# Performance work log

Hardware: AMD Instinct MI355X
Metric: run time of the kernel (lower is better)

Reference implementation:

```python
import jax, jax.numpy as jnp
import numpy as np

B, T = 16, 8192
L, RC, DC, SC, EC, E, NC = 16, 32, 32, 256, 256, 100, 256


def conv1d(x, w, b, dilation=1):
    # x: [B, Cin, T], w: [Cout, Cin, K], b: [Cout]
    y = jax.lax.conv_general_dilated(
        x, w, window_strides=(1,), padding='VALID',
        rhs_dilation=(dilation,), dimension_numbers=('NCH', 'OIH', 'NCH'))
    return y + b[None, :, None]


def setup_inputs() -> dict:
    key = jax.random.key(0)
    ks = jax.random.split(key, 32)
    n = lambda k, shp: (jax.random.normal(k, shp) * 0.1).astype(jnp.float32)
    return dict(
        tokens=jax.random.randint(ks[0], (B, T), 0, NC),
        emb=n(ks[1], (NC, E)),
        init_w=n(ks[2], (RC, E, 1)), init_b=n(ks[3], (RC,)),
        dil_w=n(ks[4], (L, DC, RC, 2)), dil_b=n(ks[5], (L, DC)),
        filt_w=n(ks[6], (L, DC, DC, 2)), filt_b=n(ks[7], (L, DC)),
        gate_w=n(ks[8], (L, DC, DC, 2)), gate_b=n(ks[9], (L, DC)),
        res_w=n(ks[10], (L, RC, DC, 1)), res_b=n(ks[11], (L, RC)),
        skip_w=n(ks[12], (L, SC, DC, 1)), skip_b=n(ks[13], (L, SC)),
        end1_w=n(ks[14], (EC, SC, 1)), end1_b=n(ks[15], (EC,)),
        end2_w=n(ks[16], (EC, EC, 1)), end2_b=n(ks[17], (EC,)),
        fc1_w=n(ks[18], (128, 256)), fc1_b=n(ks[19], (128,)),
        fc2_w=n(ks[20], (128, 128)), fc2_b=n(ks[21], (128,)),
        fc3_w=n(ks[22], (64, 128)), fc3_b=n(ks[23], (64,)),
        fc4_w=n(ks[24], (NC, 64)), fc4_b=n(ks[25], (NC,)),
    )


def reference(tokens, emb, init_w, init_b, dil_w, dil_b, filt_w, filt_b,
              gate_w, gate_b, res_w, res_b, skip_w, skip_b,
              end1_w, end1_b, end2_w, end2_b,
              fc1_w, fc1_b, fc2_w, fc2_b, fc3_w, fc3_b, fc4_w, fc4_b):
    x = emb[tokens]                     # [B, T, E]
    x = jnp.transpose(x, (0, 2, 1))     # [B, E, T]
    x = conv1d(x, init_w, init_b)       # [B, RC, T]
    skip = None
    for i in range(L):
        d = 2 ** (i % 4)                # dilation resets each block of 4 layers
        xp = jnp.pad(x, ((0, 0), (0, 0), (d + 1, 0)))        # left pad d+1
        residual = conv1d(xp, dil_w[i], dil_b[i], dilation=d)  # [B, DC, T+1]
        f = jnp.tanh(conv1d(residual, filt_w[i], filt_b[i]))   # [B, DC, T]
        g = jax.nn.sigmoid(conv1d(residual, gate_w[i], gate_b[i]))
        x = f * g
        skip = conv1d(x, skip_w[i], skip_b[i])   # overwritten each layer (source bug, kept faithful)
        x = conv1d(x, res_w[i], res_b[i]) + residual[:, :, :-1]
    h = jax.nn.relu(conv1d(jax.nn.relu(skip), end1_w, end1_b))
    h = conv1d(h, end2_w, end2_b)       # [B, EC, T]
    h = h[:, :, -1]                     # [B, 256] last timestep only
    h = jax.nn.relu(h @ fc1_w.T + fc1_b)
    h = jax.nn.relu(h @ fc2_w.T + fc2_b)
    h = jax.nn.relu(h @ fc3_w.T + fc3_b)
    out = h @ fc4_w.T + fc4_b           # [B, NC]
    return out
```

## Files before the change

### kernel.cpp

```cpp
#include <hip/hip_runtime.h>


#define BB 16
#define TT 8192
#define LL 16
#define W0 77
#define NT 256

typedef __attribute__((ext_vector_type(8)))  short short8;
typedef __attribute__((ext_vector_type(16))) float float16;

#define MFMA_B16(a, b, c) __builtin_amdgcn_mfma_f32_32x32x16_bf16(a, b, c, 0, 0, 0)

__device__ __forceinline__ short f2bs(float f) {
  union { float ff; unsigned u; } v; v.ff = f;
  unsigned u = v.u;
  return (short)((u + 0x7FFFu + ((u >> 16) & 1u)) >> 16);
}
__device__ __forceinline__ float b2f(short h) {
  union { unsigned u; float f; } v;
  v.u = ((unsigned)(unsigned short)h) << 16; return v.f;
}
__device__ __forceinline__ float fast_sigmoid(float x) {
  return 1.f / (1.f + __expf(-x));
}
__device__ __forceinline__ float fast_tanh(float x) {
  return 2.f / (1.f + __expf(-2.f * x)) - 1.f;
}

__device__ __forceinline__ void afrag2(const short* src, int row, int kh, short8* out) {
  #pragma unroll
  for (int h = 0; h < 2; h++)
    out[h] = *(const short8*)&src[row * 32 + 16 * h + 8 * kh];
}
__device__ __forceinline__ void bfragL(const short* bw, int mat, int n, int kh, short8* out) {
  #pragma unroll
  for (int h = 0; h < 2; h++)
    out[h] = *(const short8*)&bw[((mat * 2 + h) * 64 + n * 2 + kh) * 8];
}

__global__ __launch_bounds__(NT) void wavenet_kernel(
    const int* __restrict__ tokens,
    const float* __restrict__ emb,
    const float* __restrict__ init_w, const float* __restrict__ init_b,
    const float* __restrict__ dil_w,  const float* __restrict__ dil_b,
    const float* __restrict__ filt_w, const float* __restrict__ filt_b,
    const float* __restrict__ gate_w, const float* __restrict__ gate_b,
    const float* __restrict__ res_w,  const float* __restrict__ res_b,
    const float* __restrict__ skip_w, const float* __restrict__ skip_b,
    const float* __restrict__ end1_w, const float* __restrict__ end1_b,
    const float* __restrict__ end2_w, const float* __restrict__ end2_b,
    const float* __restrict__ fc1_w,  const float* __restrict__ fc1_b,
    const float* __restrict__ fc2_w,  const float* __restrict__ fc2_b,
    const float* __restrict__ fc3_w,  const float* __restrict__ fc3_b,
    const float* __restrict__ fc4_w,  const float* __restrict__ fc4_b,
    float* __restrict__ out)
{
  __shared__ __align__(16) short bfw[2][7168];
  __shared__ float bias2[2][128];
  __shared__ float resbuf[76 * 32];
  __shared__ __align__(16) short xbuf_bf[W0 * 32];
  __shared__ __align__(16) short resbuf_bf[76 * 32];
  __shared__ __align__(16) short xmid_bf[76 * 32];
  __shared__ int   tok[W0];
  __shared__ float vecA[256], vecB[256];

  const int b    = blockIdx.x;
  const int tid  = threadIdx.x;
  const int lane = tid & 63;
  const int wv   = tid >> 6;
  const int m    = lane & 31;
  const int kh   = lane >> 5;
  const int g    = tid >> 5;
  const int cc   = tid & 31;

  float pw[7][4];
  float pb[4];

  float* iwT = (float*)&bfw[1][0];

  if (tid < W0) tok[tid] = tokens[b * TT + (TT - 1 - tid)];
  for (int idx = tid; idx < 100 * 32; idx += NT) {
    int e = idx >> 5, c2 = idx & 31;
    iwT[idx] = init_w[c2 * 100 + e];
  }
  if (tid < 32) vecA[tid] = init_b[tid];

  #pragma unroll
  for (int q = 0; q < 4; q++) {
    int rc = g + 8 * q;
    int base = cc * 32 + rc;
    pw[0][q] = dil_w[base * 2 + 0];
    pw[1][q] = dil_w[base * 2 + 1];
    pw[2][q] = filt_w[base * 2 + 0];
    pw[3][q] = filt_w[base * 2 + 1];
    pw[4][q] = gate_w[base * 2 + 0];
    pw[5][q] = gate_w[base * 2 + 1];
    pw[6][q] = res_w[base];
  }
  if (tid < 32) {
    pb[0] = dil_b[tid]; pb[1] = filt_b[tid];
    pb[2] = gate_b[tid]; pb[3] = res_b[tid];
  }
  __syncthreads();

  {
    const float bc = vecA[cc];
    for (int base0 = 0; base0 < W0; base0 += 32) {
      float acc[4] = {bc, bc, bc, bc};
      const float* er[4];
      #pragma unroll
      for (int j = 0; j < 4; j++) {
        int u = base0 + g + 8 * j; if (u > W0 - 1) u = W0 - 1;
        er[j] = emb + tok[u] * 100;
      }
      #pragma unroll 5
      for (int eq = 0; eq < 100; eq += 4) {
        float w0 = iwT[(eq+0)*32+cc], w1 = iwT[(eq+1)*32+cc];
        float w2 = iwT[(eq+2)*32+cc], w3 = iwT[(eq+3)*32+cc];
        #pragma unroll
        for (int j = 0; j < 4; j++) {
          float4 e4 = *(const float4*)(er[j] + eq);
          acc[j] += (w0 * e4.x + w1 * e4.y) + (w2 * e4.z + w3 * e4.w);
        }
      }
      #pragma unroll
      for (int j = 0; j < 4; j++) {
        int u = base0 + g + 8 * j;
        if (u < W0) xbuf_bf[u * 32 + cc] = f2bs(acc[j]);
      }
    }
  }
  #pragma unroll
  for (int mat = 0; mat < 7; mat++)
    #pragma unroll
    for (int q = 0; q < 4; q++)
      bfw[0][((mat * 2 + (q >> 1)) * 64 + cc * 2 + (q & 1)) * 8 + g] = f2bs(pw[mat][q]);
  if (tid < 32) {
    bias2[0][tid] = pb[0]; bias2[0][32+tid] = pb[1];
    bias2[0][64+tid] = pb[2]; bias2[0][96+tid] = pb[3];
  }
  __syncthreads();

  int Win = W0;
  for (int i = 0; i < LL; i++) {
    const int d = 1 << (i & 3);
    const int Wout = Win - d - 1;
    const int T1 = (Wout + 32) >> 5;
    const int T2 = (Wout + 31) >> 5;
    const short* bw = bfw[i & 1];
    const float* bs = bias2[i & 1];

    if (i + 1 < LL) {
      const int ii = i + 1;
      #pragma unroll
      for (int q = 0; q < 4; q++) {
        int rc = g + 8 * q;
        int base = (ii * 32 + cc) * 32 + rc;
        pw[0][q] = dil_w[base * 2 + 0];
        pw[1][q] = dil_w[base * 2 + 1];
        pw[2][q] = filt_w[base * 2 + 0];
        pw[3][q] = filt_w[base * 2 + 1];
        pw[4][q] = gate_w[base * 2 + 0];
        pw[5][q] = gate_w[base * 2 + 1];
        pw[6][q] = res_w[base];
      }
      if (tid < 32) {
        pb[0] = dil_b[ii * 32 + tid]; pb[1] = filt_b[ii * 32 + tid];
        pb[2] = gate_b[ii * 32 + tid]; pb[3] = res_b[ii * 32 + tid];
      }
    }

    if (wv < T1) {
      const int R = wv * 32;
      short8 bD0[2], bD1[2];
      bfragL(bw, 0, m, kh, bD0);
      bfragL(bw, 1, m, kh, bD1);
      int vra = R + m + d; if (vra > Win - 1) vra = Win - 1;
      int vrz = R + m;     if (vrz > Win - 1) vrz = Win - 1;
      short8 aA[2], aZ[2];
      afrag2(xbuf_bf, vra, kh, aA);
      afrag2(xbuf_bf, vrz, kh, aZ);
      float16 acc;
      const float bc = bs[m];
      #pragma unroll
      for (int r = 0; r < 16; r++) acc[r] = bc;
      acc = MFMA_B16(aA[0], bD0[0], acc);
      acc = MFMA_B16(aA[1], bD0[1], acc);
      acc = MFMA_B16(aZ[0], bD1[0], acc);
      acc = MFMA_B16(aZ[1], bD1[1], acc);
      #pragma unroll
      for (int r = 0; r < 16; r++) {
        int row = (r & 3) + 8 * (r >> 2) + 4 * kh;
        int vr = R + row;
        if (vr <= Wout) {
          resbuf[vr * 32 + m]    = acc[r];
          resbuf_bf[vr * 32 + m] = f2bs(acc[r]);
        }
      }
    }
    __syncthreads();

    if (wv < T2) {
      const int R = wv * 32;
      short8 bF0[2], bF1[2], bG0[2], bG1[2];
      bfragL(bw, 2, m, kh, bF0);
      bfragL(bw, 3, m, kh, bF1);
      bfragL(bw, 4, m, kh, bG0);
      bfragL(bw, 5, m, kh, bG1);
      int r1 = R + m + 1; if (r1 > Wout) r1 = Wout;
      int r0 = R + m;     if (r0 > Wout) r0 = Wout;
      short8 a1[2], a0[2];
      afrag2(resbuf_bf, r1, kh, a1);
      afrag2(resbuf_bf, r0, kh, a0);
      float16 accF, accG;
      const float bf = bs[32 + m], bg = bs[64 + m];
      #pragma unroll
      for (int r = 0; r < 16; r++) { accF[r] = bf; accG[r] = bg; }
      accF = MFMA_B16(a1[0], bF0[0], accF);
      accF = MFMA_B16(a1[1], bF0[1], accF);
      accF = MFMA_B16(a0[0], bF1[0], accF);
      accF = MFMA_B16(a0[1], bF1[1], accF);
      accG = MFMA_B16(a1[0], bG0[0], accG);
      accG = MFMA_B16(a1[1], bG0[1], accG);
      accG = MFMA_B16(a0[0], bG1[0], accG);
      accG = MFMA_B16(a0[1], bG1[1], accG);
      #pragma unroll
      for (int r = 0; r < 16; r++) {
        int row = (r & 3) + 8 * (r >> 2) + 4 * kh;
        int uf = R + row;
        if (uf < Wout)
          xmid_bf[uf * 32 + m] = f2bs(fast_tanh(accF[r]) * fast_sigmoid(accG[r]));
      }
      asm volatile("s_waitcnt lgkmcnt(0)" ::: "memory");

      short8 bR[2];
      bfragL(bw, 6, m, kh, bR);
      int rx = R + m; if (rx > Wout - 1) rx = Wout - 1;
      short8 aX[2];
      afrag2(xmid_bf, rx, kh, aX);
      float16 accX;
      const float br = bs[96 + m];
      #pragma unroll
      for (int r = 0; r < 16; r++) {
        int row = (r & 3) + 8 * (r >> 2) + 4 * kh;
        int rr = R + row + 1; if (rr > Wout) rr = Wout;
        accX[r] = br + resbuf[rr * 32 + m];
      }
      accX = MFMA_B16(aX[0], bR[0], accX);
      accX = MFMA_B16(aX[1], bR[1], accX);
      #pragma unroll
      for (int r = 0; r < 16; r++) {
        int row = (r & 3) + 8 * (r >> 2) + 4 * kh;
        int uf = R + row;
        if (uf < Wout) xbuf_bf[uf * 32 + m] = f2bs(accX[r]);
      }
    }

    if (i + 1 < LL) {
      short* bwN = bfw[(i + 1) & 1];
      #pragma unroll
      for (int mat = 0; mat < 7; mat++)
        #pragma unroll
        for (int q = 0; q < 4; q++)
          bwN[((mat * 2 + (q >> 1)) * 64 + cc * 2 + (q & 1)) * 8 + g] = f2bs(pw[mat][q]);
      if (tid < 32) {
        float* bN = bias2[(i + 1) & 1];
        bN[tid] = pb[0]; bN[32+tid] = pb[1]; bN[64+tid] = pb[2]; bN[96+tid] = pb[3];
      }
    }
    __syncthreads();
    Win = Wout;
  }

  {
    float acc = skip_b[15 * 256 + tid];
    const float* wr = skip_w + (15 * 256 + tid) * 32;
    #pragma unroll
    for (int k = 0; k < 32; k += 4) {
      float4 w = *(const float4*)&wr[k];
      acc += (w.x * b2f(xmid_bf[k])   + w.y * b2f(xmid_bf[k+1]))
           + (w.z * b2f(xmid_bf[k+2]) + w.w * b2f(xmid_bf[k+3]));
    }
    vecA[tid] = fmaxf(acc, 0.f);
  }
  __syncthreads();
  {
    const float* wr = end1_w + tid * 256;
    float a4[4] = {0.f, 0.f, 0.f, 0.f};
    #pragma unroll 4
    for (int k = 0; k < 256; k += 16) {
      #pragma unroll
      for (int q = 0; q < 4; q++) {
        float4 w = *(const float4*)&wr[k + 4 * q];
        a4[q] += (w.x * vecA[k+4*q] + w.y * vecA[k+4*q+1]) + (w.z * vecA[k+4*q+2] + w.w * vecA[k+4*q+3]);
      }
    }
    vecB[tid] = fmaxf(end1_b[tid] + (a4[0] + a4[1]) + (a4[2] + a4[3]), 0.f);
  }
  __syncthreads();
  {
    const float* wr = end2_w + tid * 256;
    float a4[4] = {0.f, 0.f, 0.f, 0.f};
    #pragma unroll 4
    for (int k = 0; k < 256; k += 16) {
      #pragma unroll
      for (int q = 0; q < 4; q++) {
        float4 w = *(const float4*)&wr[k + 4 * q];
        a4[q] += (w.x * vecB[k+4*q] + w.y * vecB[k+4*q+1]) + (w.z * vecB[k+4*q+2] + w.w * vecB[k+4*q+3]);
      }
    }
    vecA[tid] = end2_b[tid] + (a4[0] + a4[1]) + (a4[2] + a4[3]);
  }
  __syncthreads();
  if (tid < 128) {
    const float* wr = fc1_w + tid * 256;
    float a4[4] = {0.f, 0.f, 0.f, 0.f};
    #pragma unroll 4
    for (int k = 0; k < 256; k += 16) {
      #pragma unroll
      for (int q = 0; q < 4; q++) {
        float4 w = *(const float4*)&wr[k + 4 * q];
        a4[q] += (w.x * vecA[k+4*q] + w.y * vecA[k+4*q+1]) + (w.z * vecA[k+4*q+2] + w.w * vecA[k+4*q+3]);
      }
    }
    vecB[tid] = fmaxf(fc1_b[tid] + (a4[0] + a4[1]) + (a4[2] + a4[3]), 0.f);
  }
  __syncthreads();
  if (tid < 128) {
    const float* wr = fc2_w + tid * 128;
    float a4[4] = {0.f, 0.f, 0.f, 0.f};
    #pragma unroll 2
    for (int k = 0; k < 128; k += 16) {
      #pragma unroll
      for (int q = 0; q < 4; q++) {
        float4 w = *(const float4*)&wr[k + 4 * q];
        a4[q] += (w.x * vecB[k+4*q] + w.y * vecB[k+4*q+1]) + (w.z * vecB[k+4*q+2] + w.w * vecB[k+4*q+3]);
      }
    }
    vecA[tid] = fmaxf(fc2_b[tid] + (a4[0] + a4[1]) + (a4[2] + a4[3]), 0.f);
  }
  __syncthreads();
  if (tid < 64) {
    const float* wr = fc3_w + tid * 128;
    float a4[4] = {0.f, 0.f, 0.f, 0.f};
    #pragma unroll 2
    for (int k = 0; k < 128; k += 16) {
      #pragma unroll
      for (int q = 0; q < 4; q++) {
        float4 w = *(const float4*)&wr[k + 4 * q];
        a4[q] += (w.x * vecA[k+4*q] + w.y * vecA[k+4*q+1]) + (w.z * vecA[k+4*q+2] + w.w * vecA[k+4*q+3]);
      }
    }
    vecB[tid] = fmaxf(fc3_b[tid] + (a4[0] + a4[1]) + (a4[2] + a4[3]), 0.f);
  }
  __syncthreads();
  {
    const float* wr = fc4_w + tid * 64;
    float a4[4] = {0.f, 0.f, 0.f, 0.f};
    #pragma unroll
    for (int k = 0; k < 64; k += 16) {
      #pragma unroll
      for (int q = 0; q < 4; q++) {
        float4 w = *(const float4*)&wr[k + 4 * q];
        a4[q] += (w.x * vecB[k+4*q] + w.y * vecB[k+4*q+1]) + (w.z * vecB[k+4*q+2] + w.w * vecB[k+4*q+3]);
      }
    }
    out[b * 256 + tid] = fc4_b[tid] + (a4[0] + a4[1]) + (a4[2] + a4[3]);
  }
}

extern "C" void kernel_launch(void* const* d_in, const int* in_sizes, int n_in,
                              void* d_out, int out_size, void* d_ws, size_t ws_size,
                              hipStream_t stream) {
  wavenet_kernel<<<BB, NT, 0, stream>>>(
      (const int*)d_in[0],    (const float*)d_in[1],  (const float*)d_in[2],  (const float*)d_in[3],
      (const float*)d_in[4],  (const float*)d_in[5],  (const float*)d_in[6],  (const float*)d_in[7],
      (const float*)d_in[8],  (const float*)d_in[9],  (const float*)d_in[10], (const float*)d_in[11],
      (const float*)d_in[12], (const float*)d_in[13], (const float*)d_in[14], (const float*)d_in[15],
      (const float*)d_in[16], (const float*)d_in[17], (const float*)d_in[18], (const float*)d_in[19],
      (const float*)d_in[20], (const float*)d_in[21], (const float*)d_in[22], (const float*)d_in[23],
      (const float*)d_in[24], (const float*)d_in[25], (float*)d_out);
}
```

Baseline: 216.7 us.

## Process two batch rows per block, sharing the layer-weight staging

Each 512-thread block now handles two batch elements, one per 256-thread half, with per-batch shared buffers. The per-layer weight prefetch and bf16 staging are split across both halves, so each thread loads half as many weights. The fp32 residual buffer is dropped and the residual is read back from bf16, and the tail vectors reuse the x buffer. The cost is a grid of only 8 blocks instead of 16, which roughly halves parallelism on a latency-bound kernel, plus a small precision loss in the residual path.

```diff
diff --git a/kernel.cpp b/kernel.cpp
--- a/kernel.cpp
+++ b/kernel.cpp
@@ -5,7 +5,7 @@
 #define TT 8192
 #define LL 16
 #define W0 77
-#define NT 256
+#define NT 512
 
 typedef __attribute__((ext_vector_type(8)))  short short8;
 typedef __attribute__((ext_vector_type(16))) float float16;
@@ -33,13 +33,13 @@
   for (int h = 0; h < 2; h++)
     out[h] = *(const short8*)&src[row * 32 + 16 * h + 8 * kh];
 }
-__device__ __forceinline__ void bfragL(const short* bw, int mat, int n, int kh, short8* out) {
+__device__ __forceinline__ void bfragL(const short* bw, int mat, int lane, short8* out) {
   #pragma unroll
   for (int h = 0; h < 2; h++)
-    out[h] = *(const short8*)&bw[((mat * 2 + h) * 64 + n * 2 + kh) * 8];
-}
-
-__global__ __launch_bounds__(NT) void wavenet_kernel(
+    out[h] = *(const short8*)&bw[((mat * 2 + h) * 64 + lane) * 8];
+}
+
+__global__ __launch_bounds__(NT, 2) void wavenet_kernel(
     const int* __restrict__ tokens,
     const float* __restrict__ emb,
     const float* __restrict__ init_w, const float* __restrict__ init_b,
@@ -58,45 +58,46 @@
 {
   __shared__ __align__(16) short bfw[2][7168];
   __shared__ float bias2[2][128];
-  __shared__ float resbuf[76 * 32];
-  __shared__ __align__(16) short xbuf_bf[W0 * 32];
-  __shared__ __align__(16) short resbuf_bf[76 * 32];
-  __shared__ __align__(16) short xmid_bf[76 * 32];
-  __shared__ int   tok[W0];
-  __shared__ float vecA[256], vecB[256];
-
-  const int b    = blockIdx.x;
+  __shared__ __align__(16) short xbuf_bf[2][W0 * 32];
+  __shared__ __align__(16) short resbuf_bf[2][76 * 32];
+  __shared__ __align__(16) short xmid_bf[2][76 * 32];
+  __shared__ int tok[2][W0];
+
   const int tid  = threadIdx.x;
   const int lane = tid & 63;
-  const int wv   = tid >> 6;
+  const int bat  = tid >> 8;
+  const int twv  = (tid >> 6) & 3;
   const int m    = lane & 31;
   const int kh   = lane >> 5;
-  const int g    = tid >> 5;
-  const int cc   = tid & 31;
-
-  float pw[7][4];
+  const int tid2 = tid & 255;
+  const int cc   = tid2 & 31;
+  const int g2   = tid2 >> 5;
+  const int bglob = blockIdx.x * 2 + bat;
+
+  const int qh = bat;
+  float pw[7][2];
   float pb[4];
 
   float* iwT = (float*)&bfw[1][0];
 
-  if (tid < W0) tok[tid] = tokens[b * TT + (TT - 1 - tid)];
+  if (tid2 < W0) tok[bat][tid2] = tokens[bglob * TT + (TT - 1 - tid2)];
   for (int idx = tid; idx < 100 * 32; idx += NT) {
     int e = idx >> 5, c2 = idx & 31;
     iwT[idx] = init_w[c2 * 100 + e];
   }
-  if (tid < 32) vecA[tid] = init_b[tid];
+  if (tid < 32) bias2[0][96 + tid] = init_b[tid];
 
   #pragma unroll
-  for (int q = 0; q < 4; q++) {
-    int rc = g + 8 * q;
+  for (int qi = 0; qi < 2; qi++) {
+    int rc = g2 + 8 * (2 * qh + qi);
     int base = cc * 32 + rc;
-    pw[0][q] = dil_w[base * 2 + 0];
-    pw[1][q] = dil_w[base * 2 + 1];
-    pw[2][q] = filt_w[base * 2 + 0];
-    pw[3][q] = filt_w[base * 2 + 1];
-    pw[4][q] = gate_w[base * 2 + 0];
-    pw[5][q] = gate_w[base * 2 + 1];
-    pw[6][q] = res_w[base];
+    pw[0][qi] = dil_w[base * 2 + 0];
+    pw[1][qi] = dil_w[base * 2 + 1];
+    pw[2][qi] = filt_w[base * 2 + 0];
+    pw[3][qi] = filt_w[base * 2 + 1];
+    pw[4][qi] = gate_w[base * 2 + 0];
+    pw[5][qi] = gate_w[base * 2 + 1];
+    pw[6][qi] = res_w[base];
   }
   if (tid < 32) {
     pb[0] = dil_b[tid]; pb[1] = filt_b[tid];
@@ -105,14 +106,15 @@
   __syncthreads();
 
   {
-    const float bc = vecA[cc];
+    const float bc = bias2[0][96 + cc];
+    short* xb = xbuf_bf[bat];
     for (int base0 = 0; base0 < W0; base0 += 32) {
       float acc[4] = {bc, bc, bc, bc};
       const float* er[4];
       #pragma unroll
       for (int j = 0; j < 4; j++) {
-        int u = base0 + g + 8 * j; if (u > W0 - 1) u = W0 - 1;
-        er[j] = emb + tok[u] * 100;
+        int u = base0 + g2 + 8 * j; if (u > W0 - 1) u = W0 - 1;
+        er[j] = emb + tok[bat][u] * 100;
       }
       #pragma unroll 5
       for (int eq = 0; eq < 100; eq += 4) {
@@ -126,16 +128,16 @@
       }
       #pragma unroll
       for (int j = 0; j < 4; j++) {
-        int u = base0 + g + 8 * j;
-        if (u < W0) xbuf_bf[u * 32 + cc] = f2bs(acc[j]);
+        int u = base0 + g2 + 8 * j;
+        if (u < W0) xb[u * 32 + cc] = f2bs(acc[j]);
       }
     }
   }
   #pragma unroll
   for (int mat = 0; mat < 7; mat++)
     #pragma unroll
-    for (int q = 0; q < 4; q++)
-      bfw[0][((mat * 2 + (q >> 1)) * 64 + cc * 2 + (q & 1)) * 8 + g] = f2bs(pw[mat][q]);
+    for (int qi = 0; qi < 2; qi++)
+      bfw[0][((mat * 2 + qh) * 64 + qi * 32 + cc) * 8 + g2] = f2bs(pw[mat][qi]);
   if (tid < 32) {
     bias2[0][tid] = pb[0]; bias2[0][32+tid] = pb[1];
     bias2[0][64+tid] = pb[2]; bias2[0][96+tid] = pb[3];
@@ -143,6 +145,9 @@
   __syncthreads();
 
   int Win = W0;
+  short* xb = xbuf_bf[bat];
+  short* rb = resbuf_bf[bat];
+  short* xm = xmid_bf[bat];
   for (int i = 0; i < LL; i++) {
     const int d = 1 << (i & 3);
     const int Wout = Win - d - 1;
@@ -154,16 +159,16 @@
     if (i + 1 < LL) {
       const int ii = i + 1;
       #pragma unroll
-      for (int q = 0; q < 4; q++) {
-        int rc = g + 8 * q;
+      for (int qi = 0; qi < 2; qi++) {
+        int rc = g2 + 8 * (2 * qh + qi);
         int base = (ii * 32 + cc) * 32 + rc;
-        pw[0][q] = dil_w[base * 2 + 0];
-        pw[1][q] = dil_w[base * 2 + 1];
-        pw[2][q] = filt_w[base * 2 + 0];
-        pw[3][q] = filt_w[base * 2 + 1];
-        pw[4][q] = gate_w[base * 2 + 0];
-        pw[5][q] = gate_w[base * 2 + 1];
-        pw[6][q] = res_w[base];
+        pw[0][qi] = dil_w[base * 2 + 0];
+        pw[1][qi] = dil_w[base * 2 + 1];
+        pw[2][qi] = filt_w[base * 2 + 0];
+        pw[3][qi] = filt_w[base * 2 + 1];
+        pw[4][qi] = gate_w[base * 2 + 0];
+        pw[5][qi] = gate_w[base * 2 + 1];
+        pw[6][qi] = res_w[base];
       }
       if (tid < 32) {
         pb[0] = dil_b[ii * 32 + tid]; pb[1] = filt_b[ii * 32 + tid];
@@ -171,16 +176,16 @@
       }
     }
 
-    if (wv < T1) {
-      const int R = wv * 32;
+    if (twv < T1) {
+      const int R = twv * 32;
       short8 bD0[2], bD1[2];
-      bfragL(bw, 0, m, kh, bD0);
-      bfragL(bw, 1, m, kh, bD1);
+      bfragL(bw, 0, lane, bD0);
+      bfragL(bw, 1, lane, bD1);
       int vra = R + m + d; if (vra > Win - 1) vra = Win - 1;
       int vrz = R + m;     if (vrz > Win - 1) vrz = Win - 1;
       short8 aA[2], aZ[2];
-      afrag2(xbuf_bf, vra, kh, aA);
-      afrag2(xbuf_bf, vrz, kh, aZ);
+      afrag2(xb, vra, kh, aA);
+      afrag2(xb, vrz, kh, aZ);
       float16 acc;
       const float bc = bs[m];
       #pragma unroll
@@ -193,26 +198,23 @@
       for (int r = 0; r < 16; r++) {
         int row = (r & 3) + 8 * (r >> 2) + 4 * kh;
         int vr = R + row;
-        if (vr <= Wout) {
-          resbuf[vr * 32 + m]    = acc[r];
-          resbuf_bf[vr * 32 + m] = f2bs(acc[r]);
-        }
+        if (vr <= Wout) rb[vr * 32 + m] = f2bs(acc[r]);
       }
     }
     __syncthreads();
 
-    if (wv < T2) {
-      const int R = wv * 32;
+    if (twv < T2) {
+      const int R = twv * 32;
       short8 bF0[2], bF1[2], bG0[2], bG1[2];
-      bfragL(bw, 2, m, kh, bF0);
-      bfragL(bw, 3, m, kh, bF1);
-      bfragL(bw, 4, m, kh, bG0);
-      bfragL(bw, 5, m, kh, bG1);
+      bfragL(bw, 2, lane, bF0);
+      bfragL(bw, 3, lane, bF1);
+      bfragL(bw, 4, lane, bG0);
+      bfragL(bw, 5, lane, bG1);
       int r1 = R + m + 1; if (r1 > Wout) r1 = Wout;
       int r0 = R + m;     if (r0 > Wout) r0 = Wout;
       short8 a1[2], a0[2];
-      afrag2(resbuf_bf, r1, kh, a1);
-      afrag2(resbuf_bf, r0, kh, a0);
+      afrag2(rb, r1, kh, a1);
+      afrag2(rb, r0, kh, a0);
       float16 accF, accG;
       const float bf = bs[32 + m], bg = bs[64 + m];
       #pragma unroll
@@ -230,22 +232,22 @@
         int row = (r & 3) + 8 * (r >> 2) + 4 * kh;
         int uf = R + row;
         if (uf < Wout)
-          xmid_bf[uf * 32 + m] = f2bs(fast_tanh(accF[r]) * fast_sigmoid(accG[r]));
+          xm[uf * 32 + m] = f2bs(fast_tanh(accF[r]) * fast_sigmoid(accG[r]));
       }
       asm volatile("s_waitcnt lgkmcnt(0)" ::: "memory");
 
       short8 bR[2];
-      bfragL(bw, 6, m, kh, bR);
+      bfragL(bw, 6, lane, bR);
       int rx = R + m; if (rx > Wout - 1) rx = Wout - 1;
       short8 aX[2];
-      afrag2(xmid_bf, rx, kh, aX);
+      afrag2(xm, rx, kh, aX);
       float16 accX;
       const float br = bs[96 + m];
       #pragma unroll
       for (int r = 0; r < 16; r++) {
         int row = (r & 3) + 8 * (r >> 2) + 4 * kh;
         int rr = R + row + 1; if (rr > Wout) rr = Wout;
-        accX[r] = br + resbuf[rr * 32 + m];
+        accX[r] = br + b2f(rb[rr * 32 + m]);
       }
       accX = MFMA_B16(aX[0], bR[0], accX);
       accX = MFMA_B16(aX[1], bR[1], accX);
@@ -253,7 +255,7 @@
       for (int r = 0; r < 16; r++) {
         int row = (r & 3) + 8 * (r >> 2) + 4 * kh;
         int uf = R + row;
-        if (uf < Wout) xbuf_bf[uf * 32 + m] = f2bs(accX[r]);
+        if (uf < Wout) xb[uf * 32 + m] = f2bs(accX[r]);
       }
     }
 
@@ -262,8 +264,8 @@
       #pragma unroll
       for (int mat = 0; mat < 7; mat++)
         #pragma unroll
-        for (int q = 0; q < 4; q++)
-          bwN[((mat * 2 + (q >> 1)) * 64 + cc * 2 + (q & 1)) * 8 + g] = f2bs(pw[mat][q]);
+        for (int qi = 0; qi < 2; qi++)
+          bwN[((mat * 2 + qh) * 64 + qi * 32 + cc) * 8 + g2] = f2bs(pw[mat][qi]);
       if (tid < 32) {
         float* bN = bias2[(i + 1) & 1];
         bN[tid] = pb[0]; bN[32+tid] = pb[1]; bN[64+tid] = pb[2]; bN[96+tid] = pb[3];
@@ -273,20 +275,23 @@
     Win = Wout;
   }
 
-  {
-    float acc = skip_b[15 * 256 + tid];
-    const float* wr = skip_w + (15 * 256 + tid) * 32;
+  float* vecA = (float*)&xbuf_bf[bat][0];
+  float* vecB = vecA + 256;
+  {
+    float acc = skip_b[15 * 256 + tid2];
+    const float* wr = skip_w + (15 * 256 + tid2) * 32;
+    float s = 0.f;
     #pragma unroll
     for (int k = 0; k < 32; k += 4) {
       float4 w = *(const float4*)&wr[k];
-      acc += (w.x * b2f(xmid_bf[k])   + w.y * b2f(xmid_bf[k+1]))
-           + (w.z * b2f(xmid_bf[k+2]) + w.w * b2f(xmid_bf[k+3]));
-    }
-    vecA[tid] = fmaxf(acc, 0.f);
-  }
-  __syncthreads();
-  {
-    const float* wr = end1_w + tid * 256;
+      s += (w.x * b2f(xm[k]) + w.y * b2f(xm[k+1])) + (w.z * b2f(xm[k+2]) + w.w * b2f(xm[k+3]));
+    }
+    __syncthreads();
+    vecA[tid2] = fmaxf(acc + s, 0.f);
+  }
+  __syncthreads();
+  {
+    const float* wr = end1_w + tid2 * 256;
     float a4[4] = {0.f, 0.f, 0.f, 0.f};
     #pragma unroll 4
     for (int k = 0; k < 256; k += 16) {
@@ -296,11 +301,12 @@
         a4[q] += (w.x * vecA[k+4*q] + w.y * vecA[k+4*q+1]) + (w.z * vecA[k+4*q+2] + w.w * vecA[k+4*q+3]);
       }
     }
-    vecB[tid] = fmaxf(end1_b[tid] + (a4[0] + a4[1]) + (a4[2] + a4[3]), 0.f);
-  }
-  __syncthreads();
-  {
-    const float* wr = end2_w + tid * 256;
+    vecB[tid2] = fmaxf(end1_b[tid2] + (a4[0] + a4[1]) + (a4[2] + a4[3]), 0.f);
+  }
+  __syncthreads();
+  float h2;
+  {
+    const float* wr = end2_w + tid2 * 256;
     float a4[4] = {0.f, 0.f, 0.f, 0.f};
     #pragma unroll 4
     for (int k = 0; k < 256; k += 16) {
@@ -310,11 +316,13 @@
         a4[q] += (w.x * vecB[k+4*q] + w.y * vecB[k+4*q+1]) + (w.z * vecB[k+4*q+2] + w.w * vecB[k+4*q+3]);
       }
     }
-    vecA[tid] = end2_b[tid] + (a4[0] + a4[1]) + (a4[2] + a4[3]);
-  }
-  __syncthreads();
-  if (tid < 128) {
-    const float* wr = fc1_w + tid * 256;
+    h2 = end2_b[tid2] + (a4[0] + a4[1]) + (a4[2] + a4[3]);
+  }
+  __syncthreads();
+  vecA[tid2] = h2;
+  __syncthreads();
+  if (tid2 < 128) {
+    const float* wr = fc1_w + tid2 * 256;
     float a4[4] = {0.f, 0.f, 0.f, 0.f};
     #pragma unroll 4
     for (int k = 0; k < 256; k += 16) {
@@ -324,11 +332,11 @@
         a4[q] += (w.x * vecA[k+4*q] + w.y * vecA[k+4*q+1]) + (w.z * vecA[k+4*q+2] + w.w * vecA[k+4*q+3]);
       }
     }
-    vecB[tid] = fmaxf(fc1_b[tid] + (a4[0] + a4[1]) + (a4[2] + a4[3]), 0.f);
-  }
-  __syncthreads();
-  if (tid < 128) {
-    const float* wr = fc2_w + tid * 128;
+    vecB[tid2] = fmaxf(fc1_b[tid2] + (a4[0] + a4[1]) + (a4[2] + a4[3]), 0.f);
+  }
+  __syncthreads();
+  if (tid2 < 128) {
+    const float* wr = fc2_w + tid2 * 128;
     float a4[4] = {0.f, 0.f, 0.f, 0.f};
     #pragma unroll 2
     for (int k = 0; k < 128; k += 16) {
@@ -338,11 +346,11 @@
         a4[q] += (w.x * vecB[k+4*q] + w.y * vecB[k+4*q+1]) + (w.z * vecB[k+4*q+2] + w.w * vecB[k+4*q+3]);
       }
     }
-    vecA[tid] = fmaxf(fc2_b[tid] + (a4[0] + a4[1]) + (a4[2] + a4[3]), 0.f);
-  }
-  __syncthreads();
-  if (tid < 64) {
-    const float* wr = fc3_w + tid * 128;
+    vecA[tid2] = fmaxf(fc2_b[tid2] + (a4[0] + a4[1]) + (a4[2] + a4[3]), 0.f);
+  }
+  __syncthreads();
+  if (tid2 < 64) {
+    const float* wr = fc3_w + tid2 * 128;
     float a4[4] = {0.f, 0.f, 0.f, 0.f};
     #pragma unroll 2
     for (int k = 0; k < 128; k += 16) {
@@ -352,11 +360,11 @@
         a4[q] += (w.x * vecA[k+4*q] + w.y * vecA[k+4*q+1]) + (w.z * vecA[k+4*q+2] + w.w * vecA[k+4*q+3]);
       }
     }
-    vecB[tid] = fmaxf(fc3_b[tid] + (a4[0] + a4[1]) + (a4[2] + a4[3]), 0.f);
-  }
-  __syncthreads();
-  {
-    const float* wr = fc4_w + tid * 64;
+    vecB[tid2] = fmaxf(fc3_b[tid2] + (a4[0] + a4[1]) + (a4[2] + a4[3]), 0.f);
+  }
+  __syncthreads();
+  {
+    const float* wr = fc4_w + tid2 * 64;
     float a4[4] = {0.f, 0.f, 0.f, 0.f};
     #pragma unroll
     for (int k = 0; k < 64; k += 16) {
@@ -366,14 +374,14 @@
         a4[q] += (w.x * vecB[k+4*q] + w.y * vecB[k+4*q+1]) + (w.z * vecB[k+4*q+2] + w.w * vecB[k+4*q+3]);
       }
     }
-    out[b * 256 + tid] = fc4_b[tid] + (a4[0] + a4[1]) + (a4[2] + a4[3]);
+    out[bglob * 256 + tid2] = fc4_b[tid2] + (a4[0] + a4[1]) + (a4[2] + a4[3]);
   }
 }
 
 extern "C" void kernel_launch(void* const* d_in, const int* in_sizes, int n_in,
                               void* d_out, int out_size, void* d_ws, size_t ws_size,
                               hipStream_t stream) {
-  wavenet_kernel<<<BB, NT, 0, stream>>>(
+  wavenet_kernel<<<BB / 2, NT, 0, stream>>>(
       (const int*)d_in[0],    (const float*)d_in[1],  (const float*)d_in[2],  (const float*)d_in[3],
       (const float*)d_in[4],  (const float*)d_in[5],  (const float*)d_in[6],  (const float*)d_in[7],
       (const float*)d_in[8],  (const float*)d_in[9],  (const float*)d_in[10], (const float*)d_in[11],
```

After: 257.1 us. +18.6%, slower.

## Use warp specialization: one wave computes layers while others stage next weights

Applied to the files above, without the earlier changes.

The layer loop now runs all MFMA work on wave 0 with the weight fragments held in registers. Waves 1-3 convert and stage the next layer's weights into the double-buffered LDS. The initial embedding 1x1 convolution moves from scalar FMAs to MFMA over a bf16-staged embedding tile, and the residual buffer is kept only in bf16 inside a shared pool. This reduces to one barrier per layer and overlaps weight loading with compute. The cost is serializing up to three row tiles on a single wave and a small precision loss from the bf16 residual.

```diff
diff --git a/kernel.cpp b/kernel.cpp
--- a/kernel.cpp
+++ b/kernel.cpp
@@ -29,17 +29,37 @@
 }
 
 __device__ __forceinline__ void afrag2(const short* src, int row, int kh, short8* out) {
-  #pragma unroll
-  for (int h = 0; h < 2; h++)
-    out[h] = *(const short8*)&src[row * 32 + 16 * h + 8 * kh];
-}
-__device__ __forceinline__ void bfragL(const short* bw, int mat, int n, int kh, short8* out) {
-  #pragma unroll
-  for (int h = 0; h < 2; h++)
-    out[h] = *(const short8*)&bw[((mat * 2 + h) * 64 + n * 2 + kh) * 8];
-}
-
-__global__ __launch_bounds__(NT) void wavenet_kernel(
+  out[0] = *(const short8*)&src[row * 32 + 8 * kh];
+  out[1] = *(const short8*)&src[row * 32 + 16 + 8 * kh];
+}
+
+__device__ __forceinline__ void stage_weights(
+    int li, short* dst,
+    const float* dil_w, const float* filt_w, const float* gate_w, const float* res_w,
+    int t0, int nthr)
+{
+  for (int cid = t0; cid < 896; cid += nthr) {
+    int mat = cid >> 7;
+    int rem = cid & 127;
+    int h = rem >> 6, ln = rem & 63;
+    int n = ln & 31, k2 = ln >> 5;
+    int base = (li * 32 + n) * 32 + 16 * h + 8 * k2;
+    short8 v;
+    if (mat == 6) {
+      const float* p = res_w + base;
+      #pragma unroll
+      for (int j = 0; j < 8; j++) v[j] = f2bs(p[j]);
+    } else {
+      const float* w = (mat < 2) ? dil_w : (mat < 4) ? filt_w : gate_w;
+      const float* p = w + base * 2 + (mat & 1);
+      #pragma unroll
+      for (int j = 0; j < 8; j++) v[j] = f2bs(p[2 * j]);
+    }
+    *(short8*)&dst[((mat * 2 + h) * 64 + ln) * 8] = v;
+  }
+}
+
+__global__ __launch_bounds__(NT, 1) void wavenet_kernel(
     const int* __restrict__ tokens,
     const float* __restrict__ emb,
     const float* __restrict__ init_w, const float* __restrict__ init_b,
@@ -58,220 +78,197 @@
 {
   __shared__ __align__(16) short bfw[2][7168];
   __shared__ float bias2[2][128];
-  __shared__ float resbuf[76 * 32];
-  __shared__ __align__(16) short xbuf_bf[W0 * 32];
-  __shared__ __align__(16) short resbuf_bf[76 * 32];
-  __shared__ __align__(16) short xmid_bf[76 * 32];
-  __shared__ int   tok[W0];
+  __shared__ __align__(16) short xbuf[W0 * 32];
+  __shared__ __align__(16) short pool[8624];
+  __shared__ int tok[W0];
   __shared__ float vecA[256], vecB[256];
 
-  const int b    = blockIdx.x;
+  short* rb = pool;
+  short* xm = pool + 2432;
+
   const int tid  = threadIdx.x;
   const int lane = tid & 63;
   const int wv   = tid >> 6;
   const int m    = lane & 31;
   const int kh   = lane >> 5;
-  const int g    = tid >> 5;
-  const int cc   = tid & 31;
-
-  float pw[7][4];
-  float pb[4];
-
-  float* iwT = (float*)&bfw[1][0];
+  const int b    = blockIdx.x;
 
   if (tid < W0) tok[tid] = tokens[b * TT + (TT - 1 - tid)];
-  for (int idx = tid; idx < 100 * 32; idx += NT) {
-    int e = idx >> 5, c2 = idx & 31;
-    iwT[idx] = init_w[c2 * 100 + e];
-  }
-  if (tid < 32) vecA[tid] = init_b[tid];
-
-  #pragma unroll
-  for (int q = 0; q < 4; q++) {
-    int rc = g + 8 * q;
-    int base = cc * 32 + rc;
-    pw[0][q] = dil_w[base * 2 + 0];
-    pw[1][q] = dil_w[base * 2 + 1];
-    pw[2][q] = filt_w[base * 2 + 0];
-    pw[3][q] = filt_w[base * 2 + 1];
-    pw[4][q] = gate_w[base * 2 + 0];
-    pw[5][q] = gate_w[base * 2 + 1];
-    pw[6][q] = res_w[base];
-  }
-  if (tid < 32) {
-    pb[0] = dil_b[tid]; pb[1] = filt_b[tid];
-    pb[2] = gate_b[tid]; pb[3] = res_b[tid];
-  }
-  __syncthreads();
-
-  {
-    const float bc = vecA[cc];
-    for (int base0 = 0; base0 < W0; base0 += 32) {
-      float acc[4] = {bc, bc, bc, bc};
-      const float* er[4];
-      #pragma unroll
-      for (int j = 0; j < 4; j++) {
-        int u = base0 + g + 8 * j; if (u > W0 - 1) u = W0 - 1;
-        er[j] = emb + tok[u] * 100;
-      }
-      #pragma unroll 5
-      for (int eq = 0; eq < 100; eq += 4) {
-        float w0 = iwT[(eq+0)*32+cc], w1 = iwT[(eq+1)*32+cc];
-        float w2 = iwT[(eq+2)*32+cc], w3 = iwT[(eq+3)*32+cc];
-        #pragma unroll
-        for (int j = 0; j < 4; j++) {
-          float4 e4 = *(const float4*)(er[j] + eq);
-          acc[j] += (w0 * e4.x + w1 * e4.y) + (w2 * e4.z + w3 * e4.w);
-        }
-      }
-      #pragma unroll
-      for (int j = 0; j < 4; j++) {
-        int u = base0 + g + 8 * j;
-        if (u < W0) xbuf_bf[u * 32 + cc] = f2bs(acc[j]);
-      }
-    }
-  }
-  #pragma unroll
-  for (int mat = 0; mat < 7; mat++)
+  __syncthreads();
+
+  for (int cid = tid; cid < 77 * 14; cid += NT) {
+    int u = cid / 14, s = cid % 14;
+    const float* er = emb + tok[u] * 100 + s * 8;
+    short8 v;
+    if (s < 12) {
+      #pragma unroll
+      for (int j = 0; j < 8; j++) v[j] = f2bs(er[j]);
+    } else if (s == 12) {
+      #pragma unroll
+      for (int j = 0; j < 4; j++) v[j] = f2bs(er[j]);
+      #pragma unroll
+      for (int j = 4; j < 8; j++) v[j] = 0;
+    } else {
+      #pragma unroll
+      for (int j = 0; j < 8; j++) v[j] = 0;
+    }
+    *(short8*)&pool[u * 112 + s * 8] = v;
+  }
+  stage_weights(0, bfw[0], dil_w, filt_w, gate_w, res_w, tid, NT);
+  if (tid < 128) {
+    const float* bsrc = (tid < 32) ? dil_b : (tid < 64) ? filt_b : (tid < 96) ? gate_b : res_b;
+    bias2[0][tid] = bsrc[tid & 31];
+  }
+  __syncthreads();
+
+  if (wv == 0) {
+    short8 bi[7];
     #pragma unroll
-    for (int q = 0; q < 4; q++)
-      bfw[0][((mat * 2 + (q >> 1)) * 64 + cc * 2 + (q & 1)) * 8 + g] = f2bs(pw[mat][q]);
-  if (tid < 32) {
-    bias2[0][tid] = pb[0]; bias2[0][32+tid] = pb[1];
-    bias2[0][64+tid] = pb[2]; bias2[0][96+tid] = pb[3];
-  }
-  __syncthreads();
+    for (int s = 0; s < 7; s++) {
+      const float* p = init_w + m * 100 + s * 16 + kh * 8;
+      short8 v;
+      if (s < 6) {
+        #pragma unroll
+        for (int j = 0; j < 8; j++) v[j] = f2bs(p[j]);
+      } else if (kh == 0) {
+        #pragma unroll
+        for (int j = 0; j < 4; j++) v[j] = f2bs(p[j]);
+        #pragma unroll
+        for (int j = 4; j < 8; j++) v[j] = 0;
+      } else {
+        #pragma unroll
+        for (int j = 0; j < 8; j++) v[j] = 0;
+      }
+      bi[s] = v;
+    }
+    const float binit = init_b[m];
+    int u = 0;
+    #pragma unroll
+    for (int t = 0; t < 3; t++) {
+      int R = t * 32;
+      u = R + m; if (u > 76) u = 76;
+      float16 acc;
+      #pragma unroll
+      for (int r = 0; r < 16; r++) acc[r] = binit;
+      #pragma unroll
+      for (int s = 0; s < 7; s++) {
+        short8 a = *(const short8*)&pool[u * 112 + s * 16 + kh * 8];
+        acc = MFMA_B16(a, bi[s], acc);
+      }
+      #pragma unroll
+      for (int r = 0; r < 16; r++) {
+        int row = (r & 3) + 8 * (r >> 2) + 4 * kh;
+        int uu = R + row;
+        if (uu < W0) xbuf[uu * 32 + m] = f2bs(acc[r]);
+      }
+    }
+  }
 
   int Win = W0;
   for (int i = 0; i < LL; i++) {
+    __syncthreads();
     const int d = 1 << (i & 3);
     const int Wout = Win - d - 1;
-    const int T1 = (Wout + 32) >> 5;
-    const int T2 = (Wout + 31) >> 5;
-    const short* bw = bfw[i & 1];
-    const float* bs = bias2[i & 1];
-
-    if (i + 1 < LL) {
-      const int ii = i + 1;
-      #pragma unroll
-      for (int q = 0; q < 4; q++) {
-        int rc = g + 8 * q;
-        int base = (ii * 32 + cc) * 32 + rc;
-        pw[0][q] = dil_w[base * 2 + 0];
-        pw[1][q] = dil_w[base * 2 + 1];
-        pw[2][q] = filt_w[base * 2 + 0];
-        pw[3][q] = filt_w[base * 2 + 1];
-        pw[4][q] = gate_w[base * 2 + 0];
-        pw[5][q] = gate_w[base * 2 + 1];
-        pw[6][q] = res_w[base];
-      }
-      if (tid < 32) {
-        pb[0] = dil_b[ii * 32 + tid]; pb[1] = filt_b[ii * 32 + tid];
-        pb[2] = gate_b[ii * 32 + tid]; pb[3] = res_b[ii * 32 + tid];
-      }
-    }
-
-    if (wv < T1) {
-      const int R = wv * 32;
-      short8 bD0[2], bD1[2];
-      bfragL(bw, 0, m, kh, bD0);
-      bfragL(bw, 1, m, kh, bD1);
-      int vra = R + m + d; if (vra > Win - 1) vra = Win - 1;
-      int vrz = R + m;     if (vrz > Win - 1) vrz = Win - 1;
-      short8 aA[2], aZ[2];
-      afrag2(xbuf_bf, vra, kh, aA);
-      afrag2(xbuf_bf, vrz, kh, aZ);
-      float16 acc;
-      const float bc = bs[m];
-      #pragma unroll
-      for (int r = 0; r < 16; r++) acc[r] = bc;
-      acc = MFMA_B16(aA[0], bD0[0], acc);
-      acc = MFMA_B16(aA[1], bD0[1], acc);
-      acc = MFMA_B16(aZ[0], bD1[0], acc);
-      acc = MFMA_B16(aZ[1], bD1[1], acc);
-      #pragma unroll
-      for (int r = 0; r < 16; r++) {
-        int row = (r & 3) + 8 * (r >> 2) + 4 * kh;
-        int vr = R + row;
-        if (vr <= Wout) {
-          resbuf[vr * 32 + m]    = acc[r];
-          resbuf_bf[vr * 32 + m] = f2bs(acc[r]);
+    if (wv == 0) {
+      const short* bw = bfw[i & 1];
+      const float* bs = bias2[i & 1];
+      short8 BW[7][2];
+      #pragma unroll
+      for (int mat = 0; mat < 7; mat++)
+        #pragma unroll
+        for (int h = 0; h < 2; h++)
+          BW[mat][h] = *(const short8*)&bw[((mat * 2 + h) * 64 + lane) * 8];
+      const int T1 = (Wout + 32) >> 5;
+      const int T2 = (Wout + 31) >> 5;
+
+      for (int t = 0; t < T1; t++) {
+        int R = t * 32;
+        int vra = R + m + d; if (vra > Win - 1) vra = Win - 1;
+        int vrz = R + m;     if (vrz > Win - 1) vrz = Win - 1;
+        short8 aA[2], aZ[2];
+        afrag2(xbuf, vra, kh, aA);
+        afrag2(xbuf, vrz, kh, aZ);
+        float16 acc;
+        const float bc = bs[m];
+        #pragma unroll
+        for (int r = 0; r < 16; r++) acc[r] = bc;
+        acc = MFMA_B16(aA[0], BW[0][0], acc);
+        acc = MFMA_B16(aA[1], BW[0][1], acc);
+        acc = MFMA_B16(aZ[0], BW[1][0], acc);
+        acc = MFMA_B16(aZ[1], BW[1][1], acc);
+        #pragma unroll
+        for (int r = 0; r < 16; r++) {
+          int row = (r & 3) + 8 * (r >> 2) + 4 * kh;
+          int vr = R + row;
+          if (vr <= Wout) rb[vr * 32 + m] = f2bs(acc[r]);
         }
       }
-    }
-    __syncthreads();
-
-    if (wv < T2) {
-      const int R = wv * 32;
-      short8 bF0[2], bF1[2], bG0[2], bG1[2];
-      bfragL(bw, 2, m, kh, bF0);
-      bfragL(bw, 3, m, kh, bF1);
-      bfragL(bw, 4, m, kh, bG0);
-      bfragL(bw, 5, m, kh, bG1);
-      int r1 = R + m + 1; if (r1 > Wout) r1 = Wout;
-      int r0 = R + m;     if (r0 > Wout) r0 = Wout;
-      short8 a1[2], a0[2];
-      afrag2(resbuf_bf, r1, kh, a1);
-      afrag2(resbuf_bf, r0, kh, a0);
-      float16 accF, accG;
-      const float bf = bs[32 + m], bg = bs[64 + m];
-      #pragma unroll
-      for (int r = 0; r < 16; r++) { accF[r] = bf; accG[r] = bg; }
-      accF = MFMA_B16(a1[0], bF0[0], accF);
-      accF = MFMA_B16(a1[1], bF0[1], accF);
-      accF = MFMA_B16(a0[0], bF1[0], accF);
-      accF = MFMA_B16(a0[1], bF1[1], accF);
-      accG = MFMA_B16(a1[0], bG0[0], accG);
-      accG = MFMA_B16(a1[1], bG0[1], accG);
-      accG = MFMA_B16(a0[0], bG1[0], accG);
-      accG = MFMA_B16(a0[1], bG1[1], accG);
-      #pragma unroll
-      for (int r = 0; r < 16; r++) {
-        int row = (r & 3) + 8 * (r >> 2) + 4 * kh;
-        int uf = R + row;
-        if (uf < Wout)
-          xmid_bf[uf * 32 + m] = f2bs(fast_tanh(accF[r]) * fast_sigmoid(accG[r]));
-      }
       asm volatile("s_waitcnt lgkmcnt(0)" ::: "memory");
 
-      short8 bR[2];
-      bfragL(bw, 6, m, kh, bR);
-      int rx = R + m; if (rx > Wout - 1) rx = Wout - 1;
-      short8 aX[2];
-      afrag2(xmid_bf, rx, kh, aX);
-      float16 accX;
-      const float br = bs[96 + m];
-      #pragma unroll
-      for (int r = 0; r < 16; r++) {
-        int row = (r & 3) + 8 * (r >> 2) + 4 * kh;
-        int rr = R + row + 1; if (rr > Wout) rr = Wout;
-        accX[r] = br + resbuf[rr * 32 + m];
-      }
-      accX = MFMA_B16(aX[0], bR[0], accX);
-      accX = MFMA_B16(aX[1], bR[1], accX);
-      #pragma unroll
-      for (int r = 0; r < 16; r++) {
-        int row = (r & 3) + 8 * (r >> 2) + 4 * kh;
-        int uf = R + row;
-        if (uf < Wout) xbuf_bf[uf * 32 + m] = f2bs(accX[r]);
-      }
-    }
-
-    if (i + 1 < LL) {
-      short* bwN = bfw[(i + 1) & 1];
-      #pragma unroll
-      for (int mat = 0; mat < 7; mat++)
-        #pragma unroll
-        for (int q = 0; q < 4; q++)
-          bwN[((mat * 2 + (q >> 1)) * 64 + cc * 2 + (q & 1)) * 8 + g] = f2bs(pw[mat][q]);
-      if (tid < 32) {
-        float* bN = bias2[(i + 1) & 1];
-        bN[tid] = pb[0]; bN[32+tid] = pb[1]; bN[64+tid] = pb[2]; bN[96+tid] = pb[3];
-      }
-    }
-    __syncthreads();
+      for (int t = 0; t < T2; t++) {
+        int R = t * 32;
+        int r1 = R + m + 1; if (r1 > Wout) r1 = Wout;
+        int r0 = R + m;     if (r0 > Wout) r0 = Wout;
+        short8 a1[2], a0[2];
+        afrag2(rb, r1, kh, a1);
+        afrag2(rb, r0, kh, a0);
+        float16 accF, accG;
+        const float bf = bs[32 + m], bg = bs[64 + m];
+        #pragma unroll
+        for (int r = 0; r < 16; r++) { accF[r] = bf; accG[r] = bg; }
+        accF = MFMA_B16(a1[0], BW[2][0], accF);
+        accF = MFMA_B16(a1[1], BW[2][1], accF);
+        accF = MFMA_B16(a0[0], BW[3][0], accF);
+        accF = MFMA_B16(a0[1], BW[3][1], accF);
+        accG = MFMA_B16(a1[0], BW[4][0], accG);
+        accG = MFMA_B16(a1[1], BW[4][1], accG);
+        accG = MFMA_B16(a0[0], BW[5][0], accG);
+        accG = MFMA_B16(a0[1], BW[5][1], accG);
+        #pragma unroll
+        for (int r = 0; r < 16; r++) {
+          int row = (r & 3) + 8 * (r >> 2) + 4 * kh;
+          int uf = R + row;
+          if (uf < Wout)
+            xm[uf * 32 + m] = f2bs(fast_tanh(accF[r]) * fast_sigmoid(accG[r]));
+        }
+      }
+      asm volatile("s_waitcnt lgkmcnt(0)" ::: "memory");
+
+      for (int t = 0; t < T2; t++) {
+        int R = t * 32;
+        int rx = R + m; if (rx > Wout - 1) rx = Wout - 1;
+        short8 aX[2];
+        afrag2(xm, rx, kh, aX);
+        float16 accX;
+        const float br = bs[96 + m];
+        #pragma unroll
+        for (int r = 0; r < 16; r++) {
+          int row = (r & 3) + 8 * (r >> 2) + 4 * kh;
+          int rr = R + row + 1; if (rr > Wout) rr = Wout;
+          accX[r] = br + b2f(rb[rr * 32 + m]);
+        }
+        accX = MFMA_B16(aX[0], BW[6][0], accX);
+        accX = MFMA_B16(aX[1], BW[6][1], accX);
+        #pragma unroll
+        for (int r = 0; r < 16; r++) {
+          int row = (r & 3) + 8 * (r >> 2) + 4 * kh;
+          int uf = R + row;
+          if (uf < Wout) xbuf[uf * 32 + m] = f2bs(accX[r]);
+        }
+      }
+      asm volatile("s_waitcnt lgkmcnt(0)" ::: "memory");
+    } else if (i + 1 < LL) {
+      stage_weights(i + 1, bfw[(i + 1) & 1], dil_w, filt_w, gate_w, res_w,
+                    tid - 64, 192);
+      int idx = tid - 64;
+      if (idx < 128) {
+        const float* bsrc = (idx < 32) ? dil_b : (idx < 64) ? filt_b : (idx < 96) ? gate_b : res_b;
+        bias2[(i + 1) & 1][idx] = bsrc[(i + 1) * 32 + (idx & 31)];
+      }
+    }
     Win = Wout;
   }
+  __syncthreads();
 
   {
     float acc = skip_b[15 * 256 + tid];
@@ -279,8 +276,7 @@
     #pragma unroll
     for (int k = 0; k < 32; k += 4) {
       float4 w = *(const float4*)&wr[k];
-      acc += (w.x * b2f(xmid_bf[k])   + w.y * b2f(xmid_bf[k+1]))
-           + (w.z * b2f(xmid_bf[k+2]) + w.w * b2f(xmid_bf[k+3]));
+      acc += (w.x * b2f(xm[k]) + w.y * b2f(xm[k+1])) + (w.z * b2f(xm[k+2]) + w.w * b2f(xm[k+3]));
     }
     vecA[tid] = fmaxf(acc, 0.f);
   }
@@ -299,6 +295,7 @@
     vecB[tid] = fmaxf(end1_b[tid] + (a4[0] + a4[1]) + (a4[2] + a4[3]), 0.f);
   }
   __syncthreads();
+  float h2;
   {
     const float* wr = end2_w + tid * 256;
     float a4[4] = {0.f, 0.f, 0.f, 0.f};
@@ -310,8 +307,10 @@
         a4[q] += (w.x * vecB[k+4*q] + w.y * vecB[k+4*q+1]) + (w.z * vecB[k+4*q+2] + w.w * vecB[k+4*q+3]);
       }
     }
-    vecA[tid] = end2_b[tid] + (a4[0] + a4[1]) + (a4[2] + a4[3]);
-  }
+    h2 = end2_b[tid] + (a4[0] + a4[1]) + (a4[2] + a4[3]);
+  }
+  __syncthreads();
+  vecA[tid] = h2;
   __syncthreads();
   if (tid < 128) {
     const float* wr = fc1_w + tid * 256;
```

Result: slower. 228.9 us (+5.6%).
